# Optimization experiments

Measured on AMD Instinct MI355X. Metric: run time of the kernel, lower is better.

## Reference

```python
import math
import jax, jax.numpy as jnp
import numpy as np

B, H, S, D = 8, 16, 1024, 64

def setup_inputs() -> dict:
    key = jax.random.key(0)
    kq, kk, kv, km = jax.random.split(key, 4)
    query = jax.random.normal(kq, (B, H, S, D), dtype=jnp.float32)
    k_ = jax.random.normal(kk, (B, H, S, D), dtype=jnp.float32)
    value = jax.random.normal(kv, (B, H, S, D), dtype=jnp.float32)
    mask = jax.random.randint(km, (B, 1, S, S), 0, 2).astype(jnp.bool_)
    return {"query": query, "key": k_, "value": value, "mask": mask}

def reference(query, key, value, mask) -> jnp.ndarray:
    dk = query.shape[-1]
    # scores: [B,H,S,S]
    scores = jnp.einsum("bhqd,bhkd->bhqk", query, key) / math.sqrt(dk)
    scores = jnp.where(mask, scores, jnp.float32(-1e9))
    attention = jax.nn.softmax(scores, axis=-1)
    # log(sigmoid(v)) computed stably, then exp of the weighted sum
    logsig_v = jax.nn.log_sigmoid(value)  # [B,H,S,D]
    return jnp.exp(jnp.einsum("bhqk,bhkd->bhqd", attention, logsig_v))
```

## Files before the change

kernel.cpp:

```cpp
#include <hip/hip_runtime.h>

typedef _Float16 half8  __attribute__((ext_vector_type(8)));
typedef _Float16 half4v __attribute__((ext_vector_type(4)));
typedef _Float16 half2v __attribute__((ext_vector_type(2)));
typedef float    f32x16 __attribute__((ext_vector_type(16)));
typedef float    f32x4v __attribute__((ext_vector_type(4)));

namespace {
constexpr int kB = 8, kH = 16, kS = 1024, kD = 64;
constexpr int QT  = 128;
constexpr int KT  = 64;
constexpr int NKT = kS / KT;
constexpr int KST = 72;
constexpr size_t KH_OFF = 0;
constexpr size_t VT_OFF = (size_t)kB * kH * kS * kD * 2;
constexpr size_t MB_OFF = VT_OFF * 2;
constexpr size_t WS_NEED = MB_OFF + (size_t)kB * kS * (kS / 32) * 4;
}

__device__ __forceinline__ float logsig(float x) {
  return fminf(x, 0.f) - __logf(1.f + __expf(-fabsf(x)));
}

__global__ __launch_bounds__(256, 4)
void pre_kernel(const float* __restrict__ K, const float* __restrict__ V,
                const int* __restrict__ M, _Float16* __restrict__ Kh,
                _Float16* __restrict__ Vt, unsigned* __restrict__ Mb) {
  const int blk = blockIdx.x, t = threadIdx.x;
  if (blk < 8192) {
    const size_t idx = ((size_t)blk * 256 + t) * 4;
    f32x4v x = *(const f32x4v*)(K + idx);
    half4v o;
    #pragma unroll
    for (int j = 0; j < 4; ++j) o[j] = (_Float16)x[j];
    *(half4v*)(Kh + idx) = o;
  } else if (blk < 10240) {
    __shared__ _Float16 T[64][72];
    const int bb = blk - 8192;
    const int bh = bb >> 4, ktt = bb & 15;
    const int key = t >> 2, dc = (t & 3) << 4;
    const float* vp = V + (((size_t)bh * kS + ktt * KT + key)) * kD + dc;
    #pragma unroll
    for (int i = 0; i < 4; ++i) {
      f32x4v x = *(const f32x4v*)(vp + 4 * i);
      #pragma unroll
      for (int j = 0; j < 4; ++j) T[dc + 4 * i + j][key] = (_Float16)logsig(x[j]);
    }
    __syncthreads();
    const int d = t >> 2, kc = (t & 3) << 4;
    half8 r0 = *(const half8*)&T[d][kc];
    half8 r1 = *(const half8*)&T[d][kc + 8];
    _Float16* op = Vt + ((size_t)bh * kD + d) * kS + ktt * KT + kc;
    *(half8*)op = r0;
    *(half8*)(op + 8) = r1;
  } else {
    const int wi = (blk - 10240) * 256 + t;
    const int row = wi >> 5;
    const int wrd = wi & 31;
    const int* mp = M + (size_t)row * kS + wrd * 32;
    unsigned bits = 0;
    #pragma unroll
    for (int i = 0; i < 8; ++i) {
      const int4 v = *(const int4*)(mp + 4 * i);
      bits |= (unsigned)(v.x & 1) << (4 * i) | (unsigned)(v.y & 1) << (4 * i + 1) |
              (unsigned)(v.z & 1) << (4 * i + 2) | (unsigned)(v.w & 1) << (4 * i + 3);
    }
    Mb[wi] = bits;
  }
}

__global__ __launch_bounds__(256, 4)
void sdpa_main(const float* __restrict__ Qg_, const _Float16* __restrict__ Kh,
               const _Float16* __restrict__ Vt, const unsigned* __restrict__ Mb,
               float* __restrict__ Og_) {
  __shared__ _Float16 Klds[KT][KST];
  __shared__ _Float16 Vlds[kD][KST];
  __shared__ _Float16 Ptl[4][32][KST];

  const int t = threadIdx.x;
  const int n   = blockIdx.x;
  const int xcd = n & 7, c = n >> 3;
  const int bh  = (xcd << 4) | (c >> 3);
  const int qblk = c & 7;
  const int b   = bh >> 4;

  const float* Qg = Qg_ + ((size_t)bh * kS + (size_t)qblk * QT) * kD;
  float* Og = Og_ + ((size_t)bh * kS + (size_t)qblk * QT) * kD;

  const int l    = t & 63;
  const int w    = t >> 6;
  const int h    = l >> 5;
  const int q31  = l & 31;
  const int qloc = w * 32 + q31;
  const int qg   = qblk * QT + qloc;

  const int skey = t >> 2;
  const int sd4  = (t & 3) << 4;
  const int vrow = t >> 2;
  const int vkc  = (t & 3) << 4;

  const _Float16* kbase = Kh + ((size_t)bh * kS + skey) * kD + sd4;
  const _Float16* vbase = Vt + ((size_t)bh * kD + vrow) * kS + vkc;
  const unsigned* mbase = Mb + ((size_t)(b * kS + qg)) * 32;

  half8 qf[4];
  {
    const float* qp = Qg + (size_t)qloc * kD + 8 * h;
    #pragma unroll
    for (int cc = 0; cc < 4; ++cc) {
      f32x4v x = *(const f32x4v*)(qp + 16 * cc);
      f32x4v y = *(const f32x4v*)(qp + 16 * cc + 4);
      half8 f;
      #pragma unroll
      for (int j = 0; j < 4; ++j) {
        f[j]     = (_Float16)(x[j] * 0.125f);
        f[j + 4] = (_Float16)(y[j] * 0.125f);
      }
      qf[cc] = f;
    }
  }

  f32x16 oacc[2];
  #pragma unroll
  for (int d = 0; d < 2; ++d) {
    #pragma unroll
    for (int i = 0; i < 16; ++i) oacc[d][i] = 0.f;
  }
  float mrun = -1e9f, lrun = 0.f;

  uint4 kreg0 = *(const uint4*)(kbase);
  uint4 kreg1 = *(const uint4*)(kbase + 8);
  uint4 vreg0 = *(const uint4*)(vbase);
  uint4 vreg1 = *(const uint4*)(vbase + 8);
  uint2 mreg  = *(const uint2*)(mbase);

  for (int kt = 0; kt < NKT; ++kt) {
    __syncthreads();

    *(uint4*)&Klds[skey][sd4]     = kreg0;
    *(uint4*)&Klds[skey][sd4 + 8] = kreg1;
    *(uint4*)&Vlds[vrow][vkc]     = vreg0;
    *(uint4*)&Vlds[vrow][vkc + 8] = vreg1;

    unsigned nib[8];
    #pragma unroll
    for (int i = 0; i < 8; ++i) {
      const unsigned wv = (i >> 2) ? mreg.y : mreg.x;
      nib[i] = (wv >> (8 * (i & 3) + 4 * h)) & 0xFu;
    }

    if (kt + 1 < NKT) {
      const size_t ko = (size_t)(kt + 1) * KT * kD;
      kreg0 = *(const uint4*)(kbase + ko);
      kreg1 = *(const uint4*)(kbase + ko + 8);
      vreg0 = *(const uint4*)(vbase + (kt + 1) * KT);
      vreg1 = *(const uint4*)(vbase + (kt + 1) * KT + 8);
      mreg  = *(const uint2*)(mbase + (kt + 1) * 2);
    }
    __syncthreads();

    f32x16 sacc[2];
    #pragma unroll
    for (int ks = 0; ks < 2; ++ks) {
      #pragma unroll
      for (int i = 0; i < 16; ++i) sacc[ks][i] = 0.f;
    }
    #pragma unroll
    for (int ks = 0; ks < 2; ++ks) {
      #pragma unroll
      for (int cc = 0; cc < 4; ++cc) {
        half8 kf = *(const half8*)&Klds[32 * ks + q31][16 * cc + 8 * h];
        sacc[ks] = __builtin_amdgcn_mfma_f32_32x32x16_f16(kf, qf[cc], sacc[ks], 0, 0, 0);
      }
    }

    float smax = -1e9f;
    #pragma unroll
    for (int ks = 0; ks < 2; ++ks) {
      #pragma unroll
      for (int m4 = 0; m4 < 4; ++m4) {
        const unsigned nb = nib[4 * ks + m4];
        #pragma unroll
        for (int r = 0; r < 4; ++r) {
          float s = sacc[ks][4 * m4 + r];
          s = (nb & (1u << r)) ? s : -1e9f;
          sacc[ks][4 * m4 + r] = s;
          smax = fmaxf(smax, s);
        }
      }
    }
    smax = fmaxf(smax, __shfl_xor(smax, 32));
    const float mnew = fmaxf(mrun, smax);
    const float corr = __expf(mrun - mnew);
    mrun = mnew;

    float psum = 0.f;
    #pragma unroll
    for (int ks = 0; ks < 2; ++ks) {
      #pragma unroll
      for (int m4 = 0; m4 < 4; ++m4) {
        float e0 = __expf(sacc[ks][4 * m4 + 0] - mnew);
        float e1 = __expf(sacc[ks][4 * m4 + 1] - mnew);
        float e2 = __expf(sacc[ks][4 * m4 + 2] - mnew);
        float e3 = __expf(sacc[ks][4 * m4 + 3] - mnew);
        psum += (e0 + e1) + (e2 + e3);
        half2v p01; p01[0] = (_Float16)e0; p01[1] = (_Float16)e1;
        half2v p23; p23[0] = (_Float16)e2; p23[1] = (_Float16)e3;
        const int key0 = 32 * ks + 8 * m4 + 4 * h;
        *(half2v*)&Ptl[w][q31][key0]     = p01;
        *(half2v*)&Ptl[w][q31][key0 + 2] = p23;
      }
    }
    psum += __shfl_xor(psum, 32);
    lrun = lrun * corr + psum;
    #pragma unroll
    for (int d = 0; d < 2; ++d) {
      #pragma unroll
      for (int i = 0; i < 16; ++i) oacc[d][i] *= corr;
    }

    half8 pf[4];
    #pragma unroll
    for (int c2 = 0; c2 < 4; ++c2)
      pf[c2] = *(const half8*)&Ptl[w][q31][16 * c2 + 8 * h];
    #pragma unroll
    for (int ds = 0; ds < 2; ++ds) {
      #pragma unroll
      for (int c2 = 0; c2 < 4; ++c2) {
        half8 vf = *(const half8*)&Vlds[32 * ds + q31][16 * c2 + 8 * h];
        oacc[ds] = __builtin_amdgcn_mfma_f32_32x32x16_f16(vf, pf[c2], oacc[ds], 0, 0, 0);
      }
    }
  }

  const float invl = 1.f / lrun;
  float* op = Og + (size_t)qloc * kD;
  #pragma unroll
  for (int ds = 0; ds < 2; ++ds) {
    #pragma unroll
    for (int m4 = 0; m4 < 4; ++m4) {
      f32x4v v;
      #pragma unroll
      for (int r = 0; r < 4; ++r)
        v[r] = __expf(oacc[ds][4 * m4 + r] * invl);
      *(f32x4v*)&op[32 * ds + 8 * m4 + 4 * h] = v;
    }
  }
}

__global__ __launch_bounds__(256, 2)
void sdpa_logsig_kernel(const float* __restrict__ Qg_, const float* __restrict__ Kg_,
                        const float* __restrict__ Vg_, const void* __restrict__ Mg_,
                        float* __restrict__ Og_) {
  __shared__ _Float16 Klds[KT][KST];
  __shared__ _Float16 Vlds[kD][KST];
  __shared__ _Float16 Ptl[4][32][KST];

  const int t = threadIdx.x;
  const int qblk = blockIdx.x;
  const int bh = blockIdx.y;
  const int b = bh >> 4;

  const float* Qg = Qg_ + ((size_t)bh * kS + (size_t)qblk * QT) * kD;
  const float* Kg = Kg_ + (size_t)bh * kS * kD;
  const float* Vg = Vg_ + (size_t)bh * kS * kD;
  float* Og = Og_ + ((size_t)bh * kS + (size_t)qblk * QT) * kD;

  const int l = t & 63, w = t >> 6, h = l >> 5, q31 = l & 31;
  const int qloc = w * 32 + q31;
  const int qg = qblk * QT + qloc;
  const int skey = t >> 2, sj = t & 3, sd4 = sj << 4;

  unsigned pacc = 0;
  {
    const unsigned* mprobe = (const unsigned*)Mg_;
    #pragma unroll
    for (int i = 0; i < 16; ++i) pacc |= mprobe[i] & 0xFFFFFF00u;
  }
  const bool mask_i32 = (pacc == 0);
  const size_t moff0 = (size_t)b * kS * kS + (size_t)qg * kS + 4 * h;

  half8 qf[4];
  {
    const float* qp = Qg + (size_t)qloc * kD + 8 * h;
    #pragma unroll
    for (int cc = 0; cc < 4; ++cc) {
      f32x4v x = *(const f32x4v*)(qp + 16 * cc);
      f32x4v y = *(const f32x4v*)(qp + 16 * cc + 4);
      half8 f;
      #pragma unroll
      for (int j = 0; j < 4; ++j) { f[j] = (_Float16)(x[j] * 0.125f); f[j + 4] = (_Float16)(y[j] * 0.125f); }
      qf[cc] = f;
    }
  }
  f32x16 oacc[2];
  #pragma unroll
  for (int d = 0; d < 2; ++d) {
    #pragma unroll
    for (int i = 0; i < 16; ++i) oacc[d][i] = 0.f;
  }
  float mrun = -1e9f, lrun = 0.f;

  for (int kt = 0; kt < NKT; ++kt) {
    __syncthreads();
    {
      const float* kp = Kg + (size_t)(kt * KT + skey) * kD + sd4;
      f32x4v a0 = *(const f32x4v*)(kp);     f32x4v a1 = *(const f32x4v*)(kp + 4);
      f32x4v a2 = *(const f32x4v*)(kp + 8); f32x4v a3 = *(const f32x4v*)(kp + 12);
      half8 h0, h1;
      #pragma unroll
      for (int j = 0; j < 4; ++j) { h0[j] = (_Float16)a0[j]; h0[j+4] = (_Float16)a1[j]; h1[j] = (_Float16)a2[j]; h1[j+4] = (_Float16)a3[j]; }
      *(half8*)&Klds[skey][sd4] = h0; *(half8*)&Klds[skey][sd4 + 8] = h1;
    }
    {
      const float* vp = Vg + (size_t)(kt * KT + skey) * kD + sd4;
      _Float16 lv[16];
      #pragma unroll
      for (int i = 0; i < 4; ++i) {
        const int cc = (i + sj) & 3;
        f32x4v xv = *(const f32x4v*)(vp + 4 * cc);
        #pragma unroll
        for (int jj = 0; jj < 4; ++jj) lv[4 * i + jj] = (_Float16)logsig(xv[jj]);
      }
      #pragma unroll
      for (int i = 0; i < 4; ++i) {
        const int cc = (i + sj) & 3;
        #pragma unroll
        for (int jj = 0; jj < 4; ++jj) Vlds[sd4 + 4 * cc + jj][skey] = lv[4 * i + jj];
      }
    }
    unsigned mq[8];
    if (mask_i32) {
      const int* mp = (const int*)Mg_ + moff0 + kt * KT;
      #pragma unroll
      for (int i = 0; i < 8; ++i) {
        const int4 mv = *(const int4*)(mp + 32 * (i >> 2) + 8 * (i & 3));
        mq[i] = (unsigned)(mv.x & 1) | ((unsigned)(mv.y & 1) << 8) |
                ((unsigned)(mv.z & 1) << 16) | ((unsigned)(mv.w & 1) << 24);
      }
    } else {
      const unsigned char* mp = (const unsigned char*)Mg_ + moff0 + kt * KT;
      #pragma unroll
      for (int i = 0; i < 8; ++i) mq[i] = *(const unsigned*)(mp + 32 * (i >> 2) + 8 * (i & 3));
    }
    __syncthreads();

    f32x16 sacc[2];
    #pragma unroll
    for (int ks = 0; ks < 2; ++ks) {
      #pragma unroll
      for (int i = 0; i < 16; ++i) sacc[ks][i] = 0.f;
    }
    #pragma unroll
    for (int ks = 0; ks < 2; ++ks) {
      #pragma unroll
      for (int cc = 0; cc < 4; ++cc) {
        half8 kf = *(const half8*)&Klds[32 * ks + q31][16 * cc + 8 * h];
        sacc[ks] = __builtin_amdgcn_mfma_f32_32x32x16_f16(kf, qf[cc], sacc[ks], 0, 0, 0);
      }
    }
    float smax = -1e9f;
    #pragma unroll
    for (int ks = 0; ks < 2; ++ks) {
      #pragma unroll
      for (int m4 = 0; m4 < 4; ++m4) {
        const unsigned mw = mq[4 * ks + m4];
        #pragma unroll
        for (int r = 0; r < 4; ++r) {
          float s = sacc[ks][4 * m4 + r];
          s = ((mw >> (8 * r)) & 0xffu) ? s : -1e9f;
          sacc[ks][4 * m4 + r] = s;
          smax = fmaxf(smax, s);
        }
      }
    }
    smax = fmaxf(smax, __shfl_xor(smax, 32));
    const float mnew = fmaxf(mrun, smax);
    const float corr = __expf(mrun - mnew);
    mrun = mnew;
    float psum = 0.f;
    #pragma unroll
    for (int ks = 0; ks < 2; ++ks) {
      #pragma unroll
      for (int m4 = 0; m4 < 4; ++m4) {
        _Float16 p0 = (_Float16)__expf(sacc[ks][4*m4+0] - mnew);
        _Float16 p1 = (_Float16)__expf(sacc[ks][4*m4+1] - mnew);
        _Float16 p2 = (_Float16)__expf(sacc[ks][4*m4+2] - mnew);
        _Float16 p3 = (_Float16)__expf(sacc[ks][4*m4+3] - mnew);
        psum += (float)p0 + (float)p1 + (float)p2 + (float)p3;
        half2v p01; p01[0] = p0; p01[1] = p1;
        half2v p23; p23[0] = p2; p23[1] = p3;
        const int key0 = 32 * ks + 8 * m4 + 4 * h;
        *(half2v*)&Ptl[w][q31][key0] = p01;
        *(half2v*)&Ptl[w][q31][key0 + 2] = p23;
      }
    }
    psum += __shfl_xor(psum, 32);
    lrun = lrun * corr + psum;
    #pragma unroll
    for (int d = 0; d < 2; ++d) {
      #pragma unroll
      for (int i = 0; i < 16; ++i) oacc[d][i] *= corr;
    }

    half8 pf[4];
    #pragma unroll
    for (int c2 = 0; c2 < 4; ++c2) pf[c2] = *(const half8*)&Ptl[w][q31][16 * c2 + 8 * h];
    #pragma unroll
    for (int ds = 0; ds < 2; ++ds) {
      #pragma unroll
      for (int c2 = 0; c2 < 4; ++c2) {
        half8 vf = *(const half8*)&Vlds[32 * ds + q31][16 * c2 + 8 * h];
        oacc[ds] = __builtin_amdgcn_mfma_f32_32x32x16_f16(vf, pf[c2], oacc[ds], 0, 0, 0);
      }
    }
  }
  const float invl = 1.f / lrun;
  float* op = Og + (size_t)qloc * kD;
  #pragma unroll
  for (int ds = 0; ds < 2; ++ds) {
    #pragma unroll
    for (int m4 = 0; m4 < 4; ++m4) {
      f32x4v v;
      #pragma unroll
      for (int r = 0; r < 4; ++r) v[r] = __expf(oacc[ds][4 * m4 + r] * invl);
      *(f32x4v*)&op[32 * ds + 8 * m4 + 4 * h] = v;
    }
  }
}

extern "C" void kernel_launch(void* const* d_in, const int* in_sizes, int n_in,
                              void* d_out, int out_size, void* d_ws, size_t ws_size,
                              hipStream_t stream) {
  const float* Q = (const float*)d_in[0];
  const float* K = (const float*)d_in[1];
  const float* V = (const float*)d_in[2];
  float* O = (float*)d_out;
  if (ws_size >= WS_NEED) {
    _Float16* Kh = (_Float16*)((char*)d_ws + KH_OFF);
    _Float16* Vt = (_Float16*)((char*)d_ws + VT_OFF);
    unsigned* Mb = (unsigned*)((char*)d_ws + MB_OFF);
    pre_kernel<<<11264, 256, 0, stream>>>(K, V, (const int*)d_in[3], Kh, Vt, Mb);
    sdpa_main<<<1024, 256, 0, stream>>>(Q, Kh, Vt, Mb, O);
  } else {
    sdpa_logsig_kernel<<<dim3(kS / QT, kB * kH), 256, 0, stream>>>(Q, K, V, d_in[3], O);
  }
}
```

Before: 224.1 us.

## Drop LDS staging, load K/V fragments directly and permute P in registers

Each wave now reads K and V MFMA fragments straight from global memory instead of staging them through shared memory with block-wide barriers. The P matrix is rearranged into the B-operand layout with v_permlane32_swap rather than a round trip through LDS. Softmax moves to exp2 with log2e folded into the Q scale, and the running-max rescale is skipped unless the new max exceeds the old by more than 8. Removing the syncthreads and LDS traffic comes at the cost of redundant global/L2 reads across the four waves and no software prefetch of the next tile.

```diff
diff --git a/kernel.cpp b/kernel.cpp
--- a/kernel.cpp
+++ b/kernel.cpp
@@ -5,6 +5,7 @@
 typedef _Float16 half2v __attribute__((ext_vector_type(2)));
 typedef float    f32x16 __attribute__((ext_vector_type(16)));
 typedef float    f32x4v __attribute__((ext_vector_type(4)));
+typedef unsigned uint4v __attribute__((ext_vector_type(4)));
 
 namespace {
 constexpr int kB = 8, kH = 16, kS = 1024, kD = 64;
@@ -20,6 +21,11 @@
 
 __device__ __forceinline__ float logsig(float x) {
   return fminf(x, 0.f) - __logf(1.f + __expf(-fabsf(x)));
+}
+
+__device__ __forceinline__ unsigned pkf16(float a, float b) {
+  half2v p; p[0] = (_Float16)a; p[1] = (_Float16)b;
+  return __builtin_bit_cast(unsigned, p);
 }
 
 __global__ __launch_bounds__(256, 4)
@@ -73,16 +79,12 @@
 void sdpa_main(const float* __restrict__ Qg_, const _Float16* __restrict__ Kh,
                const _Float16* __restrict__ Vt, const unsigned* __restrict__ Mb,
                float* __restrict__ Og_) {
-  __shared__ _Float16 Klds[KT][KST];
-  __shared__ _Float16 Vlds[kD][KST];
-  __shared__ _Float16 Ptl[4][32][KST];
-
   const int t = threadIdx.x;
-  const int n   = blockIdx.x;
-  const int xcd = n & 7, c = n >> 3;
-  const int bh  = (xcd << 4) | (c >> 3);
+  const int n    = blockIdx.x;
+  const int xcd  = n & 7, c = n >> 3;
+  const int bh   = (xcd << 4) | (c >> 3);
   const int qblk = c & 7;
-  const int b   = bh >> 4;
+  const int b    = bh >> 4;
 
   const float* Qg = Qg_ + ((size_t)bh * kS + (size_t)qblk * QT) * kD;
   float* Og = Og_ + ((size_t)bh * kS + (size_t)qblk * QT) * kD;
@@ -94,15 +96,11 @@
   const int qloc = w * 32 + q31;
   const int qg   = qblk * QT + qloc;
 
-  const int skey = t >> 2;
-  const int sd4  = (t & 3) << 4;
-  const int vrow = t >> 2;
-  const int vkc  = (t & 3) << 4;
-
-  const _Float16* kbase = Kh + ((size_t)bh * kS + skey) * kD + sd4;
-  const _Float16* vbase = Vt + ((size_t)bh * kD + vrow) * kS + vkc;
-  const unsigned* mbase = Mb + ((size_t)(b * kS + qg)) * 32;
-
+  const _Float16* kQ = Kh + ((size_t)bh * kS + q31) * kD + 8 * h;
+  const _Float16* vQ = Vt + ((size_t)bh * kD + q31) * kS + 8 * h;
+  const unsigned* mQ = Mb + ((size_t)b * kS + qg) * 32;
+
+  const float qscale = 0.125f * 1.4426950408889634f;
   half8 qf[4];
   {
     const float* qp = Qg + (size_t)qloc * kD + 8 * h;
@@ -113,8 +111,8 @@
       half8 f;
       #pragma unroll
       for (int j = 0; j < 4; ++j) {
-        f[j]     = (_Float16)(x[j] * 0.125f);
-        f[j + 4] = (_Float16)(y[j] * 0.125f);
+        f[j]     = (_Float16)(x[j] * qscale);
+        f[j + 4] = (_Float16)(y[j] * qscale);
       }
       qf[cc] = f;
     }
@@ -128,36 +126,16 @@
   }
   float mrun = -1e9f, lrun = 0.f;
 
-  uint4 kreg0 = *(const uint4*)(kbase);
-  uint4 kreg1 = *(const uint4*)(kbase + 8);
-  uint4 vreg0 = *(const uint4*)(vbase);
-  uint4 vreg1 = *(const uint4*)(vbase + 8);
-  uint2 mreg  = *(const uint2*)(mbase);
-
   for (int kt = 0; kt < NKT; ++kt) {
-    __syncthreads();
-
-    *(uint4*)&Klds[skey][sd4]     = kreg0;
-    *(uint4*)&Klds[skey][sd4 + 8] = kreg1;
-    *(uint4*)&Vlds[vrow][vkc]     = vreg0;
-    *(uint4*)&Vlds[vrow][vkc + 8] = vreg1;
-
-    unsigned nib[8];
-    #pragma unroll
-    for (int i = 0; i < 8; ++i) {
-      const unsigned wv = (i >> 2) ? mreg.y : mreg.x;
-      nib[i] = (wv >> (8 * (i & 3) + 4 * h)) & 0xFu;
-    }
-
-    if (kt + 1 < NKT) {
-      const size_t ko = (size_t)(kt + 1) * KT * kD;
-      kreg0 = *(const uint4*)(kbase + ko);
-      kreg1 = *(const uint4*)(kbase + ko + 8);
-      vreg0 = *(const uint4*)(vbase + (kt + 1) * KT);
-      vreg1 = *(const uint4*)(vbase + (kt + 1) * KT + 8);
-      mreg  = *(const uint2*)(mbase + (kt + 1) * 2);
-    }
-    __syncthreads();
+    const uint2 mreg = *(const uint2*)(mQ + kt * 2);
+
+    half8 kf[2][4];
+    #pragma unroll
+    for (int ks = 0; ks < 2; ++ks) {
+      #pragma unroll
+      for (int cc = 0; cc < 4; ++cc)
+        kf[ks][cc] = *(const half8*)(kQ + kt * 4096 + ks * 2048 + cc * 16);
+    }
 
     f32x16 sacc[2];
     #pragma unroll
@@ -168,68 +146,76 @@
     #pragma unroll
     for (int ks = 0; ks < 2; ++ks) {
       #pragma unroll
-      for (int cc = 0; cc < 4; ++cc) {
-        half8 kf = *(const half8*)&Klds[32 * ks + q31][16 * cc + 8 * h];
-        sacc[ks] = __builtin_amdgcn_mfma_f32_32x32x16_f16(kf, qf[cc], sacc[ks], 0, 0, 0);
-      }
-    }
-
-    float smax = -1e9f;
-    #pragma unroll
-    for (int ks = 0; ks < 2; ++ks) {
+      for (int cc = 0; cc < 4; ++cc)
+        sacc[ks] = __builtin_amdgcn_mfma_f32_32x32x16_f16(kf[ks][cc], qf[cc], sacc[ks], 0, 0, 0);
+    }
+
+    half8 vf[2][4];
+    #pragma unroll
+    for (int ds = 0; ds < 2; ++ds) {
+      #pragma unroll
+      for (int c2 = 0; c2 < 4; ++c2)
+        vf[ds][c2] = *(const half8*)(vQ + kt * 64 + ds * 32768 + c2 * 16);
+    }
+
+    float pmax = -1e9f;
+    #pragma unroll
+    for (int ks = 0; ks < 2; ++ks) {
+      const unsigned wv = ks ? mreg.y : mreg.x;
       #pragma unroll
       for (int m4 = 0; m4 < 4; ++m4) {
-        const unsigned nb = nib[4 * ks + m4];
+        const unsigned nb = (wv >> (8 * m4 + 4 * h)) & 0xFu;
         #pragma unroll
         for (int r = 0; r < 4; ++r) {
           float s = sacc[ks][4 * m4 + r];
           s = (nb & (1u << r)) ? s : -1e9f;
           sacc[ks][4 * m4 + r] = s;
-          smax = fmaxf(smax, s);
+          pmax = fmaxf(pmax, s);
         }
       }
     }
-    smax = fmaxf(smax, __shfl_xor(smax, 32));
-    const float mnew = fmaxf(mrun, smax);
-    const float corr = __expf(mrun - mnew);
-    mrun = mnew;
-
+    pmax = fmaxf(pmax, __shfl_xor(pmax, 32));
+
+    if (!__all(pmax <= mrun + 8.f)) {
+      const float mnew = fmaxf(mrun, pmax);
+      const float corr = __builtin_amdgcn_exp2f(mrun - mnew);
+      mrun = mnew;
+      lrun *= corr;
+      #pragma unroll
+      for (int d = 0; d < 2; ++d) {
+        #pragma unroll
+        for (int i = 0; i < 16; ++i) oacc[d][i] *= corr;
+      }
+    }
+
+    float e[2][16];
     float psum = 0.f;
     #pragma unroll
     for (int ks = 0; ks < 2; ++ks) {
       #pragma unroll
-      for (int m4 = 0; m4 < 4; ++m4) {
-        float e0 = __expf(sacc[ks][4 * m4 + 0] - mnew);
-        float e1 = __expf(sacc[ks][4 * m4 + 1] - mnew);
-        float e2 = __expf(sacc[ks][4 * m4 + 2] - mnew);
-        float e3 = __expf(sacc[ks][4 * m4 + 3] - mnew);
-        psum += (e0 + e1) + (e2 + e3);
-        half2v p01; p01[0] = (_Float16)e0; p01[1] = (_Float16)e1;
-        half2v p23; p23[0] = (_Float16)e2; p23[1] = (_Float16)e3;
-        const int key0 = 32 * ks + 8 * m4 + 4 * h;
-        *(half2v*)&Ptl[w][q31][key0]     = p01;
-        *(half2v*)&Ptl[w][q31][key0 + 2] = p23;
+      for (int i = 0; i < 16; ++i) {
+        e[ks][i] = __builtin_amdgcn_exp2f(sacc[ks][i] - mrun);
+        psum += e[ks][i];
       }
     }
     psum += __shfl_xor(psum, 32);
-    lrun = lrun * corr + psum;
-    #pragma unroll
-    for (int d = 0; d < 2; ++d) {
-      #pragma unroll
-      for (int i = 0; i < 16; ++i) oacc[d][i] *= corr;
-    }
-
-    half8 pf[4];
-    #pragma unroll
-    for (int c2 = 0; c2 < 4; ++c2)
-      pf[c2] = *(const half8*)&Ptl[w][q31][16 * c2 + 8 * h];
-    #pragma unroll
-    for (int ds = 0; ds < 2; ++ds) {
-      #pragma unroll
-      for (int c2 = 0; c2 < 4; ++c2) {
-        half8 vf = *(const half8*)&Vlds[32 * ds + q31][16 * c2 + 8 * h];
-        oacc[ds] = __builtin_amdgcn_mfma_f32_32x32x16_f16(vf, pf[c2], oacc[ds], 0, 0, 0);
-      }
+    lrun += psum;
+
+    #pragma unroll
+    for (int c2 = 0; c2 < 4; ++c2) {
+      const int ks = c2 >> 1;
+      const int ma = (2 * c2) & 3;
+      const int mb2 = (2 * c2 + 1) & 3;
+      unsigned A0 = pkf16(e[ks][4 * ma + 0],  e[ks][4 * ma + 1]);
+      unsigned A1 = pkf16(e[ks][4 * ma + 2],  e[ks][4 * ma + 3]);
+      unsigned B0 = pkf16(e[ks][4 * mb2 + 0], e[ks][4 * mb2 + 1]);
+      unsigned B1 = pkf16(e[ks][4 * mb2 + 2], e[ks][4 * mb2 + 3]);
+      asm("v_permlane32_swap_b32 %0, %1" : "+v"(A0), "+v"(B0));
+      asm("v_permlane32_swap_b32 %0, %1" : "+v"(A1), "+v"(B1));
+      uint4v pw; pw[0] = A0; pw[1] = A1; pw[2] = B0; pw[3] = B1;
+      const half8 pf = __builtin_bit_cast(half8, pw);
+      oacc[0] = __builtin_amdgcn_mfma_f32_32x32x16_f16(vf[0][c2], pf, oacc[0], 0, 0, 0);
+      oacc[1] = __builtin_amdgcn_mfma_f32_32x32x16_f16(vf[1][c2], pf, oacc[1], 0, 0, 0);
     }
   }
 
```

Measured after the change: 290.8 us. 29.7% more time.
